# Kernel optimization log

Hardware: AMD Instinct MI355X
Metric: run time of the kernel (lower is better)

The kernel has to match this reference:

```python
import jax, jax.numpy as jnp
import numpy as np

B, S, H = 8, 2048, 1024
CHUNK = 64
INTER = 2048
BASE_LR = 0.01
MAX_GRAD_NORM = 1.0
EPS = 1e-6


def rmsnorm(x, w):
    return x * jax.lax.rsqrt(jnp.mean(x * x, axis=-1, keepdims=True) + EPS) * w


def mem_fwd(params, x):
    # 2-layer MLP memory with residual: x + RMSNorm(W1 @ silu(W0 @ x))
    w0, w1, ln = params
    h = jax.nn.silu(x @ w0.T)
    y = h @ w1.T
    return x + rmsnorm(y, ln)


def forward(x, wq_w, wk_w, wv_w, q_norm_w, k_norm_w, alpha_w, theta_w, eta_w, mem_w0, mem_w1, mem_ln_w):
    Bx, Sx, Hx = x.shape
    NC = Sx // CHUNK  # seq_len divisible by chunk_size here (no padding needed)
    xc = x.reshape(Bx, NC, CHUNK, Hx)
    xf = xc.reshape(Bx, NC, CHUNK * Hx)

    # adaptive coefficients per chunk
    alpha = jax.nn.sigmoid(jnp.mean(xf @ alpha_w.T, axis=0))   # (NC, 1)
    theta = jax.nn.sigmoid(xf @ theta_w.T) * BASE_LR           # (B, NC, 1) per-sample loss weights
    eta = jax.nn.sigmoid(jnp.mean(xf @ eta_w.T, axis=0))       # (NC, 1)
    beta = 1.0 - alpha

    k = rmsnorm(jax.nn.silu(xc @ wk_w.T), k_norm_w)  # (B, NC, C, H)
    v = jax.nn.silu(xc @ wv_w.T)                     # (B, NC, C, H)

    mem0 = (mem_w0, mem_w1, mem_ln_w)
    surp0 = jax.tree_util.tree_map(jnp.zeros_like, mem0)

    def step(carry, inp):
        mem, surp = carry
        k_c, v_c, th_c, eta_c, beta_c = inp  # k_c,v_c: (B,C,H); th_c: (B,1); eta_c,beta_c: (1,)

        def loss_fn(p):
            pred = mem_fwd(p, k_c)
            return jnp.mean((v_c - pred) ** 2 * th_c[:, :, None])

        grads = jax.grad(loss_fn)(mem)
        total = jnp.sqrt(sum(jnp.sum(g * g) for g in grads))
        clip = jax.lax.stop_gradient(jnp.minimum(MAX_GRAD_NORM / (total + 1e-6), 1.0))
        new_surp = tuple(eta_c * s_ - g * clip for s_, g in zip(surp, grads))
        new_mem = tuple(beta_c * m + ns for m, ns in zip(mem, new_surp))
        return (new_mem, new_surp), None

    xs = (jnp.swapaxes(k, 0, 1), jnp.swapaxes(v, 0, 1), jnp.swapaxes(theta, 0, 1), eta, beta)
    (mem_f, _), _ = jax.lax.scan(step, (mem0, surp0), xs)

    # retrieve with final memory weights
    q = rmsnorm(jax.nn.silu(x @ wq_w.T), q_norm_w)
    return mem_fwd(mem_f, q)


def setup_inputs() -> dict:
    key = jax.random.key(0)
    ks = jax.random.split(key, 9)
    s = 0.02
    return {
        "x": jax.random.normal(ks[0], (B, S, H), jnp.float32),
        "wq_w": jax.random.normal(ks[1], (H, H), jnp.float32) * s,
        "wk_w": jax.random.normal(ks[2], (H, H), jnp.float32) * s,
        "wv_w": jax.random.normal(ks[3], (H, H), jnp.float32) * s,
        "q_norm_w": jnp.ones((H,), jnp.float32),
        "k_norm_w": jnp.ones((H,), jnp.float32),
        "alpha_w": jax.random.normal(ks[4], (1, CHUNK * H), jnp.float32) * s,
        "theta_w": jax.random.normal(ks[5], (1, CHUNK * H), jnp.float32) * s,
        "eta_w": jax.random.normal(ks[6], (1, CHUNK * H), jnp.float32) * s,
        "mem_w0": jax.random.normal(ks[7], (INTER, H), jnp.float32) * s,
        "mem_w1": jax.random.normal(ks[8], (H, INTER), jnp.float32) * s,
        "mem_ln_w": jnp.ones((H,), jnp.float32),
    }


def reference(x, wq_w, wk_w, wv_w, q_norm_w, k_norm_w, alpha_w, theta_w, eta_w, mem_w0, mem_w1, mem_ln_w):
    return forward(x, wq_w, wk_w, wv_w, q_norm_w, k_norm_w, alpha_w, theta_w, eta_w, mem_w0, mem_w1, mem_ln_w)
```

## Files before the change

kernel.cpp:

```cpp
#include <hip/hip_runtime.h>

#define HD 1024
#define ID 2048
#define NCHUNK 32
#define CHUNKSZ 64
#define NB 8
#define SEQ 2048
#define ROWS 512
#define MTOT 524288.0f
#define EPSF 1e-6f

typedef unsigned short u16;
typedef unsigned int u32;
typedef short bf16x8 __attribute__((ext_vector_type(8)));
typedef float f32x4 __attribute__((ext_vector_type(4)));

#define GATHER(r, c) ((((r) >> 6) * SEQ) + ((c) * CHUNKSZ) + ((r) & 63))

__device__ __forceinline__ float sigmoidf_(float x) { return 1.f / (1.f + expf(-x)); }
__device__ __forceinline__ float siluf_(float x)    { return x / (1.f + expf(-x)); }
__device__ __forceinline__ float silu_d_(float z)   { float sg = sigmoidf_(z); return sg * (1.f + z * (1.f - sg)); }

__device__ __forceinline__ u16 f2b(float f) {
  union { float f; u32 u; } v; v.f = f;
  return (u16)((v.u + 0x7fffu + ((v.u >> 16) & 1u)) >> 16);
}
__device__ __forceinline__ float b2f(u16 b) {
  union { u32 u; float f; } v; v.u = ((u32)b) << 16; return v.f;
}
__device__ __forceinline__ u32 pack2(float a, float b) { return (u32)f2b(a) | ((u32)f2b(b) << 16); }

__device__ __forceinline__ float block_reduce_sum(float v, float* s4) {
  #pragma unroll
  for (int off = 32; off > 0; off >>= 1) v += __shfl_down(v, off);
  int lane = threadIdx.x & 63, wid = threadIdx.x >> 6;
  if (lane == 0) s4[wid] = v;
  __syncthreads();
  float r = s4[0] + s4[1] + s4[2] + s4[3];
  __syncthreads();
  return r;
}

template<bool T>
__device__ __forceinline__ void stage64(u16* S, int srow, int c16, const uint4& r0, const uint4& r1) {
  if (!T) {
    *(uint4*)(S + srow * 72 + c16)     = r0;
    *(uint4*)(S + srow * 72 + c16 + 8) = r1;
  } else {
    const u16* e0 = (const u16*)&r0;
    const u16* e1 = (const u16*)&r1;
    #pragma unroll
    for (int e = 0; e < 8; ++e) S[(c16 + e) * 72 + srow] = e0[e];
    #pragma unroll
    for (int e = 0; e < 8; ++e) S[(c16 + 8 + e) * 72 + srow] = e1[e];
  }
}

template<bool AT, bool BT>
__device__ __forceinline__ void gemm64_db(
    f32x4 (&acc)[2][2], const u16* __restrict__ A, const u16* __restrict__ B,
    int K, int m0, int n0, int lda, int ldb, int chA, int chB,
    u16* As, u16* Bs)
{
  const int tid = threadIdx.x;
  const int lane = tid & 63, wave = tid >> 6;
  const int wr = wave >> 1, wc = wave & 1;
  const int l15 = lane & 15, q = lane >> 4;
  const int srow = tid >> 2, c16 = (tid & 3) * 16;

  const u16* Ap; size_t Astep;
  if (!AT) {
    int r = m0 + srow;
    if (chA >= 0) r = GATHER(r, chA);
    Ap = A + (size_t)r * lda + c16;
    Astep = 64;
  } else {
    Ap = A + (size_t)srow * lda + m0 + c16;
    Astep = (size_t)64 * lda;
  }
  const u16* Bp; size_t Bstep;
  if (!BT) {
    Bp = B + (size_t)(n0 + srow) * ldb + c16;
    Bstep = 64;
  } else {
    if (chB >= 0) { Bp = B + ((size_t)chB * CHUNKSZ + srow) * ldb + n0 + c16; Bstep = (size_t)SEQ * ldb; }
    else          { Bp = B + (size_t)srow * ldb + n0 + c16;                   Bstep = (size_t)64 * ldb; }
  }

  uint4 ra0 = *(const uint4*)Ap, ra1 = *(const uint4*)(Ap + 8);
  uint4 rb0 = *(const uint4*)Bp, rb1 = *(const uint4*)(Bp + 8);
  stage64<AT>(As, srow, c16, ra0, ra1);
  stage64<BT>(Bs, srow, c16, rb0, rb1);

  const int nt = K >> 6;
  int cur = 0;
  for (int t = 0; t < nt; ++t) {
    if (t + 1 < nt) {
      Ap += Astep; Bp += Bstep;
      ra0 = *(const uint4*)Ap; ra1 = *(const uint4*)(Ap + 8);
      rb0 = *(const uint4*)Bp; rb1 = *(const uint4*)(Bp + 8);
    }
    __syncthreads();
    const u16* Ac = As + cur * (64 * 72);
    const u16* Bc = Bs + cur * (64 * 72);
    #pragma unroll
    for (int ks = 0; ks < 2; ++ks) {
      bf16x8 af[2], bg[2];
      #pragma unroll
      for (int i = 0; i < 2; ++i) af[i] = *(const bf16x8*)&Ac[(wr * 32 + i * 16 + l15) * 72 + ks * 32 + q * 8];
      #pragma unroll
      for (int j = 0; j < 2; ++j) bg[j] = *(const bf16x8*)&Bc[(wc * 32 + j * 16 + l15) * 72 + ks * 32 + q * 8];
      #pragma unroll
      for (int i = 0; i < 2; ++i)
        #pragma unroll
        for (int j = 0; j < 2; ++j)
          acc[i][j] = __builtin_amdgcn_mfma_f32_16x16x32_bf16(af[i], bg[j], acc[i][j], 0, 0, 0);
    }
    if (t + 1 < nt) {
      stage64<AT>(As + (cur ^ 1) * (64 * 72), srow, c16, ra0, ra1);
      stage64<BT>(Bs + (cur ^ 1) * (64 * 72), srow, c16, rb0, rb1);
    }
    cur ^= 1;
  }
}

template<bool BT>
__device__ __forceinline__ void gemm64x8(
    f32x4 (&acc)[2][2], const u16* __restrict__ A, const u16* __restrict__ B,
    int K, int m0, int n0, int lda, int ldb, int chA, u16* As, u16* Bs)
{
  const int tid = threadIdx.x;
  const int half = tid >> 8;
  const int t2 = tid & 255;
  const int lane = tid & 63;
  const int w2 = t2 >> 6;
  const int wr = w2 >> 1, wc = w2 & 1;
  const int l15 = lane & 15, q = lane >> 4;
  const int srow = t2 >> 2, c16 = (t2 & 3) * 16;
  const int kbase = half * (K >> 1);

  int arow = m0 + srow;
  if (chA >= 0) arow = GATHER(arow, chA);
  const u16* Ap = A + (size_t)arow * lda + kbase + c16;
  const u16* Bp; size_t Bstep;
  if (!BT) { Bp = B + (size_t)(n0 + srow) * ldb + kbase + c16; Bstep = 64; }
  else     { Bp = B + (size_t)(kbase + srow) * ldb + n0 + c16; Bstep = (size_t)64 * ldb; }

  u16* Ah = As + half * (2 * 64 * 72);
  u16* Bh = Bs + half * (2 * 64 * 72);

  uint4 ra0 = *(const uint4*)Ap, ra1 = *(const uint4*)(Ap + 8);
  uint4 rb0 = *(const uint4*)Bp, rb1 = *(const uint4*)(Bp + 8);
  stage64<false>(Ah, srow, c16, ra0, ra1);
  stage64<BT>(Bh, srow, c16, rb0, rb1);

  const int nt = K >> 7;
  int cur = 0;
  for (int t = 0; t < nt; ++t) {
    if (t + 1 < nt) {
      Ap += 64; Bp += Bstep;
      ra0 = *(const uint4*)Ap; ra1 = *(const uint4*)(Ap + 8);
      rb0 = *(const uint4*)Bp; rb1 = *(const uint4*)(Bp + 8);
    }
    __syncthreads();
    const u16* Ac = Ah + cur * (64 * 72);
    const u16* Bc = Bh + cur * (64 * 72);
    #pragma unroll
    for (int ks = 0; ks < 2; ++ks) {
      bf16x8 af[2], bg[2];
      #pragma unroll
      for (int i = 0; i < 2; ++i) af[i] = *(const bf16x8*)&Ac[(wr * 32 + i * 16 + l15) * 72 + ks * 32 + q * 8];
      #pragma unroll
      for (int j = 0; j < 2; ++j) bg[j] = *(const bf16x8*)&Bc[(wc * 32 + j * 16 + l15) * 72 + ks * 32 + q * 8];
      #pragma unroll
      for (int i = 0; i < 2; ++i)
        #pragma unroll
        for (int j = 0; j < 2; ++j)
          acc[i][j] = __builtin_amdgcn_mfma_f32_16x16x32_bf16(af[i], bg[j], acc[i][j], 0, 0, 0);
    }
    if (t + 1 < nt) {
      stage64<false>(Ah + (cur ^ 1) * (64 * 72), srow, c16, ra0, ra1);
      stage64<BT>(Bh + (cur ^ 1) * (64 * 72), srow, c16, rb0, rb1);
    }
    cur ^= 1;
  }
}

__global__ __launch_bounds__(512) void gemm64_fwd(
    float* __restrict__ C, u16* __restrict__ Cb,
    const u16* __restrict__ A, const u16* __restrict__ B, int N, int K, int chunk)
{
  __shared__ __align__(16) u16 As[2 * 2 * 64 * 72];
  __shared__ __align__(16) u16 Bs[2 * 2 * 64 * 72];
  const int m0 = blockIdx.y * 64, n0 = blockIdx.x * 64;
  f32x4 acc[2][2] = {};
  gemm64x8<false>(acc, A, B, K, m0, n0, K, K, chunk, As, Bs);
  const int tid = threadIdx.x;
  const int half = tid >> 8, t2 = tid & 255;
  const int lane = tid & 63, w2 = t2 >> 6;
  const int wr = w2 >> 1, wc = w2 & 1;
  const int l15 = lane & 15, q = lane >> 4;
  float* Cm = (float*)As;
  __syncthreads();
  if (half) {
    #pragma unroll
    for (int i = 0; i < 2; ++i)
      #pragma unroll
      for (int j = 0; j < 2; ++j)
        #pragma unroll
        for (int t = 0; t < 4; ++t)
          Cm[(wr * 32 + i * 16 + q * 4 + t) * 66 + wc * 32 + j * 16 + l15] = acc[i][j][t];
  }
  __syncthreads();
  if (!half) {
    #pragma unroll
    for (int i = 0; i < 2; ++i) {
      int r = m0 + wr * 32 + i * 16 + q * 4;
      #pragma unroll
      for (int j = 0; j < 2; ++j) {
        int col = n0 + wc * 32 + j * 16 + l15;
        #pragma unroll
        for (int t = 0; t < 4; ++t) {
          float v = acc[i][j][t] + Cm[(wr * 32 + i * 16 + q * 4 + t) * 66 + wc * 32 + j * 16 + l15];
          size_t o = (size_t)(r + t) * N + col;
          C[o] = v;
          Cb[o] = f2b(siluf_(v));
        }
      }
    }
  }
}

__global__ __launch_bounds__(512) void gemm64_dh(
    u16* __restrict__ Cb, const u16* __restrict__ A, const u16* __restrict__ B,
    const float* __restrict__ Z, int N, int K)
{
  __shared__ __align__(16) u16 As[2 * 2 * 64 * 72];
  __shared__ __align__(16) u16 Bs[2 * 2 * 64 * 72];
  const int m0 = blockIdx.y * 64, n0 = blockIdx.x * 64;
  f32x4 acc[2][2] = {};
  gemm64x8<true>(acc, A, B, K, m0, n0, K, N, -1, As, Bs);
  const int tid = threadIdx.x;
  const int half = tid >> 8, t2 = tid & 255;
  const int lane = tid & 63, w2 = t2 >> 6;
  const int wr = w2 >> 1, wc = w2 & 1;
  const int l15 = lane & 15, q = lane >> 4;
  float* Cm = (float*)As;
  __syncthreads();
  if (half) {
    #pragma unroll
    for (int i = 0; i < 2; ++i)
      #pragma unroll
      for (int j = 0; j < 2; ++j)
        #pragma unroll
        for (int t = 0; t < 4; ++t)
          Cm[(wr * 32 + i * 16 + q * 4 + t) * 66 + wc * 32 + j * 16 + l15] = acc[i][j][t];
  }
  __syncthreads();
  if (!half) {
    #pragma unroll
    for (int i = 0; i < 2; ++i) {
      int r = m0 + wr * 32 + i * 16 + q * 4;
      #pragma unroll
      for (int j = 0; j < 2; ++j) {
        int col = n0 + wc * 32 + j * 16 + l15;
        #pragma unroll
        for (int t = 0; t < 4; ++t) {
          float v = acc[i][j][t] + Cm[(wr * 32 + i * 16 + q * 4 + t) * 66 + wc * 32 + j * 16 + l15];
          size_t o = (size_t)(r + t) * N + col;
          Cb[o] = f2b(v * silu_d_(Z[o]));
        }
      }
    }
  }
}

__global__ __launch_bounds__(256) void gemm_grads(
    float* __restrict__ Gw1, const u16* __restrict__ dY, const u16* __restrict__ hfw,
    float* __restrict__ Gw0, const u16* __restrict__ dH, const u16* __restrict__ kall,
    int c, const float* __restrict__ g, const float* __restrict__ y,
    const float* __restrict__ srow, float* __restrict__ Gln, float* __restrict__ nsqc)
{
  __shared__ __align__(16) u16 As[2 * 64 * 72];
  __shared__ __align__(16) u16 Bs[2 * 64 * 72];
  __shared__ float s4[4];
  int bid = blockIdx.x;
  const int tid = threadIdx.x;
  if (bid >= 1024) {
    int j = (bid - 1024) * 32 + (tid & 31);
    int rg = tid >> 5;
    float acc = 0.f;
    #pragma unroll 4
    for (int i = 0; i < 64; ++i) {
      int r = rg * 64 + i;
      size_t o = (size_t)r * HD + j;
      acc += g[o] * y[o] * srow[r];
    }
    float* part = (float*)As;
    part[rg * 32 + (tid & 31)] = acc;
    __syncthreads();
    if (tid < 32) {
      float tot = 0.f;
      #pragma unroll
      for (int k = 0; k < 8; ++k) tot += part[k * 32 + tid];
      Gln[j] = tot;
      float sq = tot * tot;
      #pragma unroll
      for (int off = 16; off > 0; off >>= 1) sq += __shfl_down(sq, off);
      if (tid == 0) atomicAdd(nsqc, sq);
    }
    return;
  }
  float* C; const u16* A; const u16* B; int N, m0, n0, lda, ldb, chB;
  if (bid < 512) { A = dY; B = hfw;  C = Gw1; N = ID; lda = HD; ldb = ID; chB = -1; m0 = (bid >> 5) * 64; n0 = (bid & 31) * 64; }
  else { bid -= 512; A = dH; B = kall; C = Gw0; N = HD; lda = ID; ldb = HD; chB = c; m0 = (bid >> 4) * 64; n0 = (bid & 15) * 64; }
  f32x4 acc[2][2] = {};
  gemm64_db<true, true>(acc, A, B, ROWS, m0, n0, lda, ldb, -1, chB, As, Bs);
  const int lane = tid & 63, wave = tid >> 6;
  const int wr = wave >> 1, wc = wave & 1;
  const int l15 = lane & 15, q = lane >> 4;
  float ssq = 0.f;
  #pragma unroll
  for (int i = 0; i < 2; ++i) {
    int r = m0 + wr * 32 + i * 16 + q * 4;
    #pragma unroll
    for (int j = 0; j < 2; ++j) {
      int col = n0 + wc * 32 + j * 16 + l15;
      #pragma unroll
      for (int t = 0; t < 4; ++t) {
        float v = acc[i][j][t];
        C[(size_t)(r + t) * N + col] = v;
        ssq += v * v;
      }
    }
  }
  float tot = block_reduce_sum(ssq, s4);
  if (tid == 0) atomicAdd(nsqc, tot);
}

__global__ __launch_bounds__(512) void gemm_y32(
    float* __restrict__ C, const u16* __restrict__ A, const u16* __restrict__ B,
    int N, int K)
{
  __shared__ __align__(16) u16 As[4 * 2 * 32 * 72];
  __shared__ __align__(16) u16 Bs[4 * 2 * 64 * 72];
  const int tid = threadIdx.x;
  const int qt = tid >> 7;
  const int t2 = tid & 127;
  const int lane = tid & 63;
  const int wc = t2 >> 6;
  const int l15 = lane & 15, q = lane >> 4;
  const int m0 = blockIdx.y * 32, n0 = blockIdx.x * 64;
  const int kbase = qt * (K >> 2);

  const int arow = t2 >> 2, ac16 = (t2 & 3) * 16;
  const int brow = t2 >> 1, bc32 = (t2 & 1) * 32;
  const u16* Ap = A + (size_t)(m0 + arow) * K + kbase + ac16;
  const u16* Bp = B + (size_t)(n0 + brow) * K + kbase + bc32;
  u16* Aq = As + qt * (2 * 32 * 72);
  u16* Bq = Bs + qt * (2 * 64 * 72);

  uint4 ra0 = *(const uint4*)Ap, ra1 = *(const uint4*)(Ap + 8);
  uint4 rb0 = *(const uint4*)Bp, rb1 = *(const uint4*)(Bp + 8);
  uint4 rb2 = *(const uint4*)(Bp + 16), rb3 = *(const uint4*)(Bp + 24);
  {
    u16* Aw = Aq + arow * 72 + ac16;
    u16* Bw = Bq + brow * 72 + bc32;
    *(uint4*)Aw = ra0; *(uint4*)(Aw + 8) = ra1;
    *(uint4*)Bw = rb0; *(uint4*)(Bw + 8) = rb1;
    *(uint4*)(Bw + 16) = rb2; *(uint4*)(Bw + 24) = rb3;
  }

  f32x4 acc[2][2] = {};
  const int nt = K >> 8;
  int cur = 0;
  for (int t = 0; t < nt; ++t) {
    if (t + 1 < nt) {
      Ap += 64; Bp += 64;
      ra0 = *(const uint4*)Ap; ra1 = *(const uint4*)(Ap + 8);
      rb0 = *(const uint4*)Bp; rb1 = *(const uint4*)(Bp + 8);
      rb2 = *(const uint4*)(Bp + 16); rb3 = *(const uint4*)(Bp + 24);
    }
    __syncthreads();
    const u16* Ac = Aq + cur * (32 * 72);
    const u16* Bc = Bq + cur * (64 * 72);
    #pragma unroll
    for (int ks = 0; ks < 2; ++ks) {
      bf16x8 af[2], bg[2];
      #pragma unroll
      for (int i = 0; i < 2; ++i) af[i] = *(const bf16x8*)&Ac[(i * 16 + l15) * 72 + ks * 32 + q * 8];
      #pragma unroll
      for (int j = 0; j < 2; ++j) bg[j] = *(const bf16x8*)&Bc[(wc * 32 + j * 16 + l15) * 72 + ks * 32 + q * 8];
      #pragma unroll
      for (int i = 0; i < 2; ++i)
        #pragma unroll
        for (int j = 0; j < 2; ++j)
          acc[i][j] = __builtin_amdgcn_mfma_f32_16x16x32_bf16(af[i], bg[j], acc[i][j], 0, 0, 0);
    }
    if (t + 1 < nt) {
      u16* Aw = Aq + (cur ^ 1) * (32 * 72) + arow * 72 + ac16;
      u16* Bw = Bq + (cur ^ 1) * (64 * 72) + brow * 72 + bc32;
      *(uint4*)Aw = ra0; *(uint4*)(Aw + 8) = ra1;
      *(uint4*)Bw = rb0; *(uint4*)(Bw + 8) = rb1;
      *(uint4*)(Bw + 16) = rb2; *(uint4*)(Bw + 24) = rb3;
    }
    cur ^= 1;
  }
  float* Cm = (float*)As;
  __syncthreads();
  if (qt) {
    #pragma unroll
    for (int i = 0; i < 2; ++i)
      #pragma unroll
      for (int j = 0; j < 2; ++j)
        #pragma unroll
        for (int t = 0; t < 4; ++t)
          Cm[((qt - 1) * 32 + i * 16 + q * 4 + t) * 66 + wc * 32 + j * 16 + l15] = acc[i][j][t];
  }
  __syncthreads();
  if (!qt) {
    #pragma unroll
    for (int i = 0; i < 2; ++i) {
      int r = m0 + i * 16 + q * 4;
      #pragma unroll
      for (int j = 0; j < 2; ++j) {
        int col = n0 + wc * 32 + j * 16 + l15;
        #pragma unroll
        for (int t = 0; t < 4; ++t) {
          float v = acc[i][j][t];
          #pragma unroll
          for (int p = 0; p < 3; ++p)
            v += Cm[(p * 32 + i * 16 + q * 4 + t) * 66 + wc * 32 + j * 16 + l15];
          C[(size_t)(r + t) * N + col] = v;
        }
      }
    }
  }
}

__device__ __forceinline__ void gemm128_core(
    f32x4 (&acc)[4][4], const u16* __restrict__ A, int lda,
    const u16* __restrict__ B, int ldb, int K, int m0, int n0,
    u16* As, u16* Bs)
{
  const int tid = threadIdx.x;
  const int lane = tid & 63, wave = tid >> 6;
  const int wr = wave >> 1, wc = wave & 1;
  const int l15 = lane & 15, q = lane >> 4;
  for (int k0 = 0; k0 < K; k0 += 32) {
    #pragma unroll
    for (int it = 0; it < 2; ++it) {
      int cid = tid + it * 256;
      int row = cid >> 2, c8 = (cid & 3) * 8;
      *(uint4*)&As[row * 40 + c8] = *(const uint4*)&A[(size_t)(m0 + row) * lda + k0 + c8];
      *(uint4*)&Bs[row * 40 + c8] = *(const uint4*)&B[(size_t)(n0 + row) * ldb + k0 + c8];
    }
    __syncthreads();
    bf16x8 af[4], bg[4];
    #pragma unroll
    for (int i = 0; i < 4; ++i) af[i] = *(const bf16x8*)&As[(wr * 64 + i * 16 + l15) * 40 + q * 8];
    #pragma unroll
    for (int j = 0; j < 4; ++j) bg[j] = *(const bf16x8*)&Bs[(wc * 64 + j * 16 + l15) * 40 + q * 8];
    #pragma unroll
    for (int i = 0; i < 4; ++i)
      #pragma unroll
      for (int j = 0; j < 4; ++j)
        acc[i][j] = __builtin_amdgcn_mfma_f32_16x16x32_bf16(af[i], bg[j], acc[i][j], 0, 0, 0);
    __syncthreads();
  }
}

__global__ __launch_bounds__(256) void gemm_qkv(
    float* __restrict__ zqC, u16* __restrict__ kC, u16* __restrict__ vC,
    const u16* __restrict__ xb, const u16* __restrict__ wk,
    const u16* __restrict__ wv, const u16* __restrict__ wq)
{
  __shared__ __align__(16) u16 As[128 * 40];
  __shared__ __align__(16) u16 Bs[128 * 40];
  int f = blockIdx.x;
  int xcd = f & 7, jj = f >> 3;
  int panel = xcd + 8 * (jj / 24);
  int w = jj % 24;
  int z = w >> 3, xt = w & 7;
  int m0 = panel * 128, n0 = xt * 128;
  const u16* B = (z == 0) ? wk : ((z == 1) ? wv : wq);
  f32x4 acc[4][4] = {};
  gemm128_core(acc, xb, HD, B, HD, HD, m0, n0, As, Bs);
  const int tid = threadIdx.x;
  const int lane = tid & 63, wave = tid >> 6;
  const int wr = wave >> 1, wc = wave & 1;
  const int l15 = lane & 15, q = lane >> 4;
  #pragma unroll
  for (int i = 0; i < 4; ++i) {
    int r = m0 + wr * 64 + i * 16 + q * 4;
    #pragma unroll
    for (int j = 0; j < 4; ++j) {
      int col = n0 + wc * 64 + j * 16 + l15;
      #pragma unroll
      for (int t = 0; t < 4; ++t) {
        float v = acc[i][j][t];
        size_t o = (size_t)(r + t) * HD + col;
        if (z == 0) kC[o] = f2b(v);
        else if (z == 1) vC[o] = f2b(siluf_(v));
        else zqC[o] = v;
      }
    }
  }
}

__global__ __launch_bounds__(256) void gemm_h(
    u16* __restrict__ hC, const u16* __restrict__ A, const u16* __restrict__ B)
{
  __shared__ __align__(16) u16 As[128 * 40];
  __shared__ __align__(16) u16 Bs[128 * 40];
  int f = blockIdx.x;
  int xcd = f & 7, jj = f >> 3;
  int panel = xcd + 8 * (jj >> 4);
  int xt = jj & 15;
  int m0 = panel * 128, n0 = xt * 128;
  f32x4 acc[4][4] = {};
  gemm128_core(acc, A, HD, B, HD, HD, m0, n0, As, Bs);
  const int tid = threadIdx.x;
  const int lane = tid & 63, wave = tid >> 6;
  const int wr = wave >> 1, wc = wave & 1;
  const int l15 = lane & 15, q = lane >> 4;
  #pragma unroll
  for (int i = 0; i < 4; ++i) {
    int r = m0 + wr * 64 + i * 16 + q * 4;
    #pragma unroll
    for (int j = 0; j < 4; ++j) {
      int col = n0 + wc * 64 + j * 16 + l15;
      #pragma unroll
      for (int t = 0; t < 4; ++t)
        hC[(size_t)(r + t) * ID + col] = f2b(siluf_(acc[i][j][t]));
    }
  }
}

__global__ __launch_bounds__(256) void gemm_y2(
    float* __restrict__ C, const u16* __restrict__ A, const u16* __restrict__ B)
{
  __shared__ __align__(16) u16 As[128 * 40];
  __shared__ __align__(16) u16 Bs[128 * 40];
  int f = blockIdx.x;
  int xcd = f & 7, jj = f >> 3;
  int panel = xcd + 8 * (jj >> 3);
  int xt = jj & 7;
  int m0 = panel * 128, n0 = xt * 128;
  f32x4 acc[4][4] = {};
  gemm128_core(acc, A, ID, B, ID, ID, m0, n0, As, Bs);
  const int tid = threadIdx.x;
  const int lane = tid & 63, wave = tid >> 6;
  const int wr = wave >> 1, wc = wave & 1;
  const int l15 = lane & 15, q = lane >> 4;
  #pragma unroll
  for (int i = 0; i < 4; ++i) {
    int r = m0 + wr * 64 + i * 16 + q * 4;
    #pragma unroll
    for (int j = 0; j < 4; ++j) {
      int col = n0 + wc * 64 + j * 16 + l15;
      #pragma unroll
      for (int t = 0; t < 4; ++t)
        C[(size_t)(r + t) * HD + col] = acc[i][j][t];
    }
  }
}

__global__ __launch_bounds__(256) void conv_f2b(u16* __restrict__ dst, const float* __restrict__ src, int n) {
  int i = (blockIdx.x * 256 + threadIdx.x) * 4;
  if (i < n) {
    float4 v = *(const float4*)&src[i];
    uint2 o; o.x = pack2(v.x, v.y); o.y = pack2(v.z, v.w);
    *(uint2*)&dst[i] = o;
  }
}

__global__ __launch_bounds__(256) void dots_kernel(
    const float* __restrict__ x, const float* __restrict__ aw,
    const float* __restrict__ tw, const float* __restrict__ ew,
    float* __restrict__ dA, float* __restrict__ dT, float* __restrict__ dE)
{
  int b = blockIdx.x >> 5, c = blockIdx.x & 31;
  const float* base = x + ((size_t)b * SEQ + (size_t)c * CHUNKSZ) * HD;
  float a = 0.f, t = 0.f, e = 0.f;
  for (int it = 0; it < 64; ++it) {
    int j = (it * 256 + threadIdx.x) * 4;
    float4 xv = *(const float4*)&base[j];
    float4 av = *(const float4*)&aw[j];
    float4 tv = *(const float4*)&tw[j];
    float4 ev = *(const float4*)&ew[j];
    a += xv.x * av.x + xv.y * av.y + xv.z * av.z + xv.w * av.w;
    t += xv.x * tv.x + xv.y * tv.y + xv.z * tv.z + xv.w * tv.w;
    e += xv.x * ev.x + xv.y * ev.y + xv.z * ev.z + xv.w * ev.w;
  }
  __shared__ float s4[4];
  a = block_reduce_sum(a, s4);
  t = block_reduce_sum(t, s4);
  e = block_reduce_sum(e, s4);
  if (threadIdx.x == 0) { dA[blockIdx.x] = a; dT[blockIdx.x] = t; dE[blockIdx.x] = e; }
}

__global__ __launch_bounds__(256) void coeff_kernel(
    const float* __restrict__ dA, const float* __restrict__ dT, const float* __restrict__ dE,
    float* __restrict__ betaA, float* __restrict__ etaA, float* __restrict__ thetaA)
{
  int t = threadIdx.x;
  if (t < 256) thetaA[t] = sigmoidf_(dT[t]) * 0.01f;
  if (t < 32) {
    float sa = 0.f, se = 0.f;
    for (int b = 0; b < NB; ++b) { sa += dA[b * 32 + t]; se += dE[b * 32 + t]; }
    betaA[t] = 1.f - sigmoidf_(sa / 8.f);
    etaA[t]  = sigmoidf_(se / 8.f);
  }
}

__global__ __launch_bounds__(256) void post_norm_kb(u16* buf, const float* __restrict__ nw)
{
  size_t off = (size_t)blockIdx.x * HD;
  float sv[4]; float ss = 0.f;
  #pragma unroll
  for (int i = 0; i < 4; ++i) {
    int j = i * 256 + threadIdx.x;
    float s = siluf_(b2f(buf[off + j]));
    sv[i] = s; ss += s * s;
  }
  __shared__ float s4[4];
  ss = block_reduce_sum(ss, s4);
  float rs = rsqrtf(ss / (float)HD + EPSF);
  #pragma unroll
  for (int i = 0; i < 4; ++i) {
    int j = i * 256 + threadIdx.x;
    buf[off + j] = f2b(sv[i] * rs * nw[j]);
  }
}

__global__ __launch_bounds__(256) void post_norm_qf(float* buf, const float* __restrict__ nw)
{
  size_t off = (size_t)blockIdx.x * HD;
  float sv[4]; float ss = 0.f;
  #pragma unroll
  for (int i = 0; i < 4; ++i) {
    int j = i * 256 + threadIdx.x;
    float s = siluf_(buf[off + j]);
    sv[i] = s; ss += s * s;
  }
  __shared__ float s4[4];
  ss = block_reduce_sum(ss, s4);
  float rs = rsqrtf(ss / (float)HD + EPSF);
  #pragma unroll
  for (int i = 0; i < 4; ++i) {
    int j = i * 256 + threadIdx.x;
    buf[off + j] = sv[i] * rs * nw[j];
  }
}

__global__ __launch_bounds__(256) void loss_grad(
    const float* __restrict__ y, const u16* __restrict__ kall, const u16* __restrict__ vall,
    const float* __restrict__ ln, const float* __restrict__ thetaA, int c,
    float* __restrict__ g, u16* __restrict__ dYbf, float* __restrict__ srow)
{
  int r = blockIdx.x;
  size_t off = (size_t)r * HD;
  size_t goff = (size_t)GATHER(r, c) * HD;
  float th = thetaA[(r >> 6) * 32 + c];
  float yv[4], lnv[4];
  float ss = 0.f;
  #pragma unroll
  for (int i = 0; i < 4; ++i) {
    int j = i * 256 + threadIdx.x;
    yv[i] = y[off + j];
    lnv[i] = ln[j];
    ss += yv[i] * yv[i];
  }
  __shared__ float s4[4];
  ss = block_reduce_sum(ss, s4);
  float s = rsqrtf(ss / (float)HD + EPSF);
  float coef = 2.f * th / MTOT;
  float gv[4]; float t = 0.f;
  #pragma unroll
  for (int i = 0; i < 4; ++i) {
    int j = i * 256 + threadIdx.x;
    float pred = b2f(kall[goff + j]) + yv[i] * s * lnv[i];
    float gg = coef * (pred - b2f(vall[goff + j]));
    gv[i] = gg;
    g[off + j] = gg;
    t += gg * lnv[i] * yv[i];
  }
  t = block_reduce_sum(t, s4);
  float c3 = s * s * s * t * (1.f / (float)HD);
  #pragma unroll
  for (int i = 0; i < 4; ++i) {
    int j = i * 256 + threadIdx.x;
    dYbf[off + j] = f2b(s * gv[i] * lnv[i] - c3 * yv[i]);
  }
  if (threadIdx.x == 0) srow[r] = s;
}

__global__ __launch_bounds__(256) void update_all(
    float* __restrict__ mw0, float* __restrict__ sw0, const float* __restrict__ g0, u16* __restrict__ w0b,
    float* __restrict__ mw1, float* __restrict__ sw1, const float* __restrict__ g1, u16* __restrict__ w1b,
    float* __restrict__ mln, float* __restrict__ sln, const float* __restrict__ gl,
    const float* __restrict__ etaA, const float* __restrict__ betaA, int c,
    const float* __restrict__ nsqc)
{
  float clip = fminf(1.0f / (sqrtf(*nsqc) + 1e-6f), 1.0f);
  float eta = etaA[c], beta = betaA[c];
  int bid = blockIdx.x;
  if (bid < 2048) {
    float* mw; float* sw; const float* g; u16* wb; size_t i0;
    if (bid < 1024) { mw = mw1; sw = sw1; g = g1; wb = w1b; i0 = (size_t)bid * 2048; }
    else            { mw = mw0; sw = sw0; g = g0; wb = w0b; i0 = (size_t)(bid - 1024) * 2048; }
    i0 += (size_t)threadIdx.x * 8;
    u16 bb[8];
    #pragma unroll
    for (int h = 0; h < 2; ++h) {
      size_t i = i0 + h * 4;
      float4 s = *(float4*)&sw[i];
      float4 gg = *(const float4*)&g[i];
      float4 m = *(float4*)&mw[i];
      s.x = eta * s.x - clip * gg.x; m.x = beta * m.x + s.x;
      s.y = eta * s.y - clip * gg.y; m.y = beta * m.y + s.y;
      s.z = eta * s.z - clip * gg.z; m.z = beta * m.z + s.z;
      s.w = eta * s.w - clip * gg.w; m.w = beta * m.w + s.w;
      *(float4*)&sw[i] = s;
      *(float4*)&mw[i] = m;
      bb[h * 4 + 0] = f2b(m.x); bb[h * 4 + 1] = f2b(m.y);
      bb[h * 4 + 2] = f2b(m.z); bb[h * 4 + 3] = f2b(m.w);
    }
    *(uint4*)&wb[i0] = *(uint4*)bb;
  } else {
    int i = threadIdx.x * 4;
    #pragma unroll
    for (int k = 0; k < 4; ++k) {
      float ns = eta * sln[i + k] - clip * gl[i + k];
      sln[i + k] = ns;
      mln[i + k] = beta * mln[i + k] + ns;
    }
  }
}

__global__ __launch_bounds__(256) void final_out_kernel(
    float* outp, const float* __restrict__ y2, const float* __restrict__ ln)
{
  size_t off = (size_t)blockIdx.x * HD;
  float qv[4], yv[4];
  float ss2 = 0.f;
  #pragma unroll
  for (int i = 0; i < 4; ++i) {
    int j = i * 256 + threadIdx.x;
    qv[i] = outp[off + j];
    yv[i] = y2[off + j];
    ss2 += yv[i] * yv[i];
  }
  __shared__ float s4[4];
  ss2 = block_reduce_sum(ss2, s4);
  float rs2 = rsqrtf(ss2 / (float)HD + EPSF);
  #pragma unroll
  for (int i = 0; i < 4; ++i) {
    int j = i * 256 + threadIdx.x;
    outp[off + j] = qv[i] + yv[i] * rs2 * ln[j];
  }
}

extern "C" void kernel_launch(void* const* d_in, const int* in_sizes, int n_in,
                              void* d_out, int out_size, void* d_ws, size_t ws_size,
                              hipStream_t stream) {
  const float* x   = (const float*)d_in[0];
  const float* wq  = (const float*)d_in[1];
  const float* wk  = (const float*)d_in[2];
  const float* wv  = (const float*)d_in[3];
  const float* qn  = (const float*)d_in[4];
  const float* kn  = (const float*)d_in[5];
  const float* aw  = (const float*)d_in[6];
  const float* tw  = (const float*)d_in[7];
  const float* ew  = (const float*)d_in[8];
  const float* w0i = (const float*)d_in[9];
  const float* w1i = (const float*)d_in[10];
  const float* lni = (const float*)d_in[11];
  float* out = (float*)d_out;

  float* p = (float*)d_ws;
  auto alloc = [&](size_t n) { n = (n + 63) & ~(size_t)63; float* r = p; p += n; return r; };
  float* memW0  = alloc((size_t)ID * HD);
  float* memW1  = alloc((size_t)HD * ID);
  float* surpW0 = alloc((size_t)ID * HD);
  float* surpW1 = alloc((size_t)HD * ID);
  float* Gw0    = alloc((size_t)ID * HD);
  float* Gw1    = alloc((size_t)HD * ID);
  float* memLn  = alloc(HD);
  float* surpLn = alloc(HD);
  float* Gln    = alloc(HD);
  float* zfw    = alloc((size_t)ROWS * ID);
  float* ybuf   = alloc((size_t)ROWS * HD);
  float* gbuf   = alloc((size_t)ROWS * HD);
  float* srow   = alloc(ROWS);
  float* dotA   = alloc(256);
  float* dotT   = alloc(256);
  float* dotE   = alloc(256);
  float* betaA  = alloc(64);
  float* etaA   = alloc(64);
  float* thetaA = alloc(256);
  float* nsq    = alloc(64);

  u16* bp = (u16*)p;
  auto balloc = [&](size_t n) { n = (n + 63) & ~(size_t)63; u16* r = bp; bp += n; return r; };
  u16* wq_bf  = balloc((size_t)HD * HD);
  u16* wk_bf  = balloc((size_t)HD * HD);
  u16* wv_bf  = balloc((size_t)HD * HD);
  u16* W0_bf  = balloc((size_t)ID * HD);
  u16* W1_bf  = balloc((size_t)HD * ID);
  u16* k_all  = balloc((size_t)NB * SEQ * HD);
  u16* v_all  = balloc((size_t)NB * SEQ * HD);
  u16* hfw_bf = balloc((size_t)ROWS * ID);
  u16* dY_bf  = balloc((size_t)ROWS * HD);
  u16* dH_bf  = balloc((size_t)ROWS * ID);
  size_t needed = (size_t)((char*)bp - (char*)d_ws);
  if (needed > ws_size) return;

  u16* x_bf = (u16*)memW0;

  conv_f2b<<<(HD * HD) / 1024, 256, 0, stream>>>(wq_bf, wq, HD * HD);
  conv_f2b<<<(HD * HD) / 1024, 256, 0, stream>>>(wk_bf, wk, HD * HD);
  conv_f2b<<<(HD * HD) / 1024, 256, 0, stream>>>(wv_bf, wv, HD * HD);
  conv_f2b<<<(ID * HD) / 1024, 256, 0, stream>>>(W0_bf, w0i, ID * HD);
  conv_f2b<<<(HD * ID) / 1024, 256, 0, stream>>>(W1_bf, w1i, HD * ID);
  conv_f2b<<<(NB * SEQ * HD) / 1024, 256, 0, stream>>>(x_bf, x, NB * SEQ * HD);
  dots_kernel<<<256, 256, 0, stream>>>(x, aw, tw, ew, dotA, dotT, dotE);
  coeff_kernel<<<1, 256, 0, stream>>>(dotA, dotT, dotE, betaA, etaA, thetaA);
  gemm_qkv<<<3072, 256, 0, stream>>>(out, k_all, v_all, x_bf, wk_bf, wv_bf, wq_bf);
  post_norm_kb<<<NB * SEQ, 256, 0, stream>>>(k_all, kn);
  post_norm_qf<<<NB * SEQ, 256, 0, stream>>>(out, qn);
  hipMemcpyAsync(memW0, w0i, (size_t)ID * HD * 4, hipMemcpyDeviceToDevice, stream);
  hipMemcpyAsync(memW1, w1i, (size_t)HD * ID * 4, hipMemcpyDeviceToDevice, stream);
  hipMemcpyAsync(memLn, lni, (size_t)HD * 4, hipMemcpyDeviceToDevice, stream);
  hipMemsetAsync(surpW0, 0, (size_t)ID * HD * 2 * 4, stream);
  hipMemsetAsync(surpLn, 0, HD * 4, stream);
  hipMemsetAsync(nsq, 0, 64 * 4, stream);

  for (int c = 0; c < NCHUNK; ++c) {
    gemm64_fwd<<<dim3(ID / 64, ROWS / 64), 512, 0, stream>>>(
        zfw, hfw_bf, k_all, W0_bf, ID, HD, c);
    gemm_y32<<<dim3(HD / 64, ROWS / 32), 512, 0, stream>>>(ybuf, hfw_bf, W1_bf, HD, ID);
    loss_grad<<<ROWS, 256, 0, stream>>>(ybuf, k_all, v_all, memLn, thetaA, c, gbuf, dY_bf, srow);
    gemm64_dh<<<dim3(ID / 64, ROWS / 64), 512, 0, stream>>>(
        dH_bf, dY_bf, W1_bf, zfw, ID, HD);
    gemm_grads<<<1056, 256, 0, stream>>>(
        Gw1, dY_bf, hfw_bf, Gw0, dH_bf, k_all, c, gbuf, ybuf, srow, Gln, nsq + c);
    update_all<<<2049, 256, 0, stream>>>(
        memW0, surpW0, Gw0, W0_bf, memW1, surpW1, Gw1, W1_bf,
        memLn, surpLn, Gln, etaA, betaA, c, nsq + c);
  }

  u16*   qb_bf = k_all;
  u16*   h_bf  = v_all;
  float* y2    = surpW0;
  conv_f2b<<<(NB * SEQ * HD) / 1024, 256, 0, stream>>>(qb_bf, out, NB * SEQ * HD);
  for (int blk = 0; blk < 2; ++blk) {
    gemm_h<<<1024, 256, 0, stream>>>(h_bf, qb_bf + (size_t)blk * 8192 * HD, W0_bf);
    gemm_y2<<<512, 256, 0, stream>>>(y2, h_bf, W1_bf);
    final_out_kernel<<<8192, 256, 0, stream>>>(out + (size_t)blk * 8192 * HD, y2, memLn);
  }
}
```

Measured before the change: 3.106 ms.

## Double-buffer 128-tile GEMM core and remap transposed staging thread layout

Replaces the single-buffered 128x128 GEMM core used by the qkv, h and y2 kernels with a register-prefetched, double-buffered LDS pipeline. This overlaps the global loads for the next K tile with the MFMA work and drops one barrier per iteration. It also changes the thread-to-element mapping in the transposed staging paths of the 64-tile GEMMs so each thread owns one k-row, which changes the LDS scatter bank pattern. LDS use doubles for the 128-tile kernels, which may lower occupancy.

After: 3.221 ms. 3.7% more time.

```diff
diff --git a/kernel.cpp b/kernel.cpp
--- a/kernel.cpp
+++ b/kernel.cpp
@@ -41,56 +41,34 @@
   return r;
 }
 
-template<bool T>
-__device__ __forceinline__ void stage64(u16* S, int srow, int c16, const uint4& r0, const uint4& r1) {
-  if (!T) {
-    *(uint4*)(S + srow * 72 + c16)     = r0;
-    *(uint4*)(S + srow * 72 + c16 + 8) = r1;
-  } else {
-    const u16* e0 = (const u16*)&r0;
-    const u16* e1 = (const u16*)&r1;
-    #pragma unroll
-    for (int e = 0; e < 8; ++e) S[(c16 + e) * 72 + srow] = e0[e];
-    #pragma unroll
-    for (int e = 0; e < 8; ++e) S[(c16 + 8 + e) * 72 + srow] = e1[e];
-  }
-}
-
-template<bool AT, bool BT>
-__device__ __forceinline__ void gemm64_db(
+__device__ __forceinline__ void gemm64_tn(
     f32x4 (&acc)[2][2], const u16* __restrict__ A, const u16* __restrict__ B,
-    int K, int m0, int n0, int lda, int ldb, int chA, int chB,
-    u16* As, u16* Bs)
+    int K, int m0, int n0, int lda, int ldb, int chB, u16* As, u16* Bs)
 {
   const int tid = threadIdx.x;
   const int lane = tid & 63, wave = tid >> 6;
   const int wr = wave >> 1, wc = wave & 1;
   const int l15 = lane & 15, q = lane >> 4;
-  const int srow = tid >> 2, c16 = (tid & 3) * 16;
-
-  const u16* Ap; size_t Astep;
-  if (!AT) {
-    int r = m0 + srow;
-    if (chA >= 0) r = GATHER(r, chA);
-    Ap = A + (size_t)r * lda + c16;
-    Astep = 64;
-  } else {
-    Ap = A + (size_t)srow * lda + m0 + c16;
-    Astep = (size_t)64 * lda;
-  }
+  const int kr = tid & 63, cg = (tid >> 6) * 16;
+
+  const u16* Ap = A + (size_t)kr * lda + m0 + cg;
+  const size_t Astep = (size_t)64 * lda;
   const u16* Bp; size_t Bstep;
-  if (!BT) {
-    Bp = B + (size_t)(n0 + srow) * ldb + c16;
-    Bstep = 64;
-  } else {
-    if (chB >= 0) { Bp = B + ((size_t)chB * CHUNKSZ + srow) * ldb + n0 + c16; Bstep = (size_t)SEQ * ldb; }
-    else          { Bp = B + (size_t)srow * ldb + n0 + c16;                   Bstep = (size_t)64 * ldb; }
-  }
+  if (chB >= 0) { Bp = B + ((size_t)chB * CHUNKSZ + kr) * ldb + n0 + cg; Bstep = (size_t)SEQ * ldb; }
+  else          { Bp = B + (size_t)kr * ldb + n0 + cg;                   Bstep = (size_t)64 * ldb; }
+
+  auto scat = [&](u16* S, const uint4& r0, const uint4& r1) {
+    const u16* e0 = (const u16*)&r0; const u16* e1 = (const u16*)&r1;
+    #pragma unroll
+    for (int e = 0; e < 8; ++e) S[(cg + e) * 72 + kr] = e0[e];
+    #pragma unroll
+    for (int e = 0; e < 8; ++e) S[(cg + 8 + e) * 72 + kr] = e1[e];
+  };
 
   uint4 ra0 = *(const uint4*)Ap, ra1 = *(const uint4*)(Ap + 8);
   uint4 rb0 = *(const uint4*)Bp, rb1 = *(const uint4*)(Bp + 8);
-  stage64<AT>(As, srow, c16, ra0, ra1);
-  stage64<BT>(Bs, srow, c16, rb0, rb1);
+  scat(As, ra0, ra1);
+  scat(Bs, rb0, rb1);
 
   const int nt = K >> 6;
   int cur = 0;
@@ -117,8 +95,8 @@
           acc[i][j] = __builtin_amdgcn_mfma_f32_16x16x32_bf16(af[i], bg[j], acc[i][j], 0, 0, 0);
     }
     if (t + 1 < nt) {
-      stage64<AT>(As + (cur ^ 1) * (64 * 72), srow, c16, ra0, ra1);
-      stage64<BT>(Bs + (cur ^ 1) * (64 * 72), srow, c16, rb0, rb1);
+      scat(As + (cur ^ 1) * (64 * 72), ra0, ra1);
+      scat(Bs + (cur ^ 1) * (64 * 72), rb0, rb1);
     }
     cur ^= 1;
   }
@@ -137,6 +115,7 @@
   const int wr = w2 >> 1, wc = w2 & 1;
   const int l15 = lane & 15, q = lane >> 4;
   const int srow = t2 >> 2, c16 = (t2 & 3) * 16;
+  const int kr = t2 & 63, cg = (t2 >> 6) * 16;
   const int kbase = half * (K >> 1);
 
   int arow = m0 + srow;
@@ -144,15 +123,32 @@
   const u16* Ap = A + (size_t)arow * lda + kbase + c16;
   const u16* Bp; size_t Bstep;
   if (!BT) { Bp = B + (size_t)(n0 + srow) * ldb + kbase + c16; Bstep = 64; }
-  else     { Bp = B + (size_t)(kbase + srow) * ldb + n0 + c16; Bstep = (size_t)64 * ldb; }
+  else     { Bp = B + (size_t)(kbase + kr) * ldb + n0 + cg;    Bstep = (size_t)64 * ldb; }
 
   u16* Ah = As + half * (2 * 64 * 72);
   u16* Bh = Bs + half * (2 * 64 * 72);
 
+  auto stA = [&](u16* S, const uint4& r0, const uint4& r1) {
+    *(uint4*)(S + srow * 72 + c16)     = r0;
+    *(uint4*)(S + srow * 72 + c16 + 8) = r1;
+  };
+  auto stB = [&](u16* S, const uint4& r0, const uint4& r1) {
+    if (!BT) {
+      *(uint4*)(S + srow * 72 + c16)     = r0;
+      *(uint4*)(S + srow * 72 + c16 + 8) = r1;
+    } else {
+      const u16* e0 = (const u16*)&r0; const u16* e1 = (const u16*)&r1;
+      #pragma unroll
+      for (int e = 0; e < 8; ++e) S[(cg + e) * 72 + kr] = e0[e];
+      #pragma unroll
+      for (int e = 0; e < 8; ++e) S[(cg + 8 + e) * 72 + kr] = e1[e];
+    }
+  };
+
   uint4 ra0 = *(const uint4*)Ap, ra1 = *(const uint4*)(Ap + 8);
   uint4 rb0 = *(const uint4*)Bp, rb1 = *(const uint4*)(Bp + 8);
-  stage64<false>(Ah, srow, c16, ra0, ra1);
-  stage64<BT>(Bh, srow, c16, rb0, rb1);
+  stA(Ah, ra0, ra1);
+  stB(Bh, rb0, rb1);
 
   const int nt = K >> 7;
   int cur = 0;
@@ -179,8 +175,8 @@
           acc[i][j] = __builtin_amdgcn_mfma_f32_16x16x32_bf16(af[i], bg[j], acc[i][j], 0, 0, 0);
     }
     if (t + 1 < nt) {
-      stage64<false>(Ah + (cur ^ 1) * (64 * 72), srow, c16, ra0, ra1);
-      stage64<BT>(Bh + (cur ^ 1) * (64 * 72), srow, c16, rb0, rb1);
+      stA(Ah + (cur ^ 1) * (64 * 72), ra0, ra1);
+      stB(Bh + (cur ^ 1) * (64 * 72), rb0, rb1);
     }
     cur ^= 1;
   }
@@ -315,7 +311,7 @@
   if (bid < 512) { A = dY; B = hfw;  C = Gw1; N = ID; lda = HD; ldb = ID; chB = -1; m0 = (bid >> 5) * 64; n0 = (bid & 31) * 64; }
   else { bid -= 512; A = dH; B = kall; C = Gw0; N = HD; lda = ID; ldb = HD; chB = c; m0 = (bid >> 4) * 64; n0 = (bid & 15) * 64; }
   f32x4 acc[2][2] = {};
-  gemm64_db<true, true>(acc, A, B, ROWS, m0, n0, lda, ldb, -1, chB, As, Bs);
+  gemm64_tn(acc, A, B, ROWS, m0, n0, lda, ldb, chB, As, Bs);
   const int lane = tid & 63, wave = tid >> 6;
   const int wr = wave >> 1, wc = wave & 1;
   const int l15 = lane & 15, q = lane >> 4;
@@ -438,7 +434,7 @@
   }
 }
 
-__device__ __forceinline__ void gemm128_core(
+__device__ __forceinline__ void gemm128_db(
     f32x4 (&acc)[4][4], const u16* __restrict__ A, int lda,
     const u16* __restrict__ B, int ldb, int K, int m0, int n0,
     u16* As, u16* Bs)
@@ -447,26 +443,50 @@
   const int lane = tid & 63, wave = tid >> 6;
   const int wr = wave >> 1, wc = wave & 1;
   const int l15 = lane & 15, q = lane >> 4;
-  for (int k0 = 0; k0 < K; k0 += 32) {
-    #pragma unroll
-    for (int it = 0; it < 2; ++it) {
-      int cid = tid + it * 256;
-      int row = cid >> 2, c8 = (cid & 3) * 8;
-      *(uint4*)&As[row * 40 + c8] = *(const uint4*)&A[(size_t)(m0 + row) * lda + k0 + c8];
-      *(uint4*)&Bs[row * 40 + c8] = *(const uint4*)&B[(size_t)(n0 + row) * ldb + k0 + c8];
+  const int row0 = tid >> 2, c8 = (tid & 3) * 8;
+
+  const u16* Ap0 = A + (size_t)(m0 + row0) * lda + c8;
+  const u16* Ap1 = Ap0 + (size_t)64 * lda;
+  const u16* Bp0 = B + (size_t)(n0 + row0) * ldb + c8;
+  const u16* Bp1 = Bp0 + (size_t)64 * ldb;
+
+  uint4 a0 = *(const uint4*)Ap0, a1 = *(const uint4*)Ap1;
+  uint4 b0 = *(const uint4*)Bp0, b1 = *(const uint4*)Bp1;
+  *(uint4*)&As[row0 * 40 + c8] = a0;
+  *(uint4*)&As[(row0 + 64) * 40 + c8] = a1;
+  *(uint4*)&Bs[row0 * 40 + c8] = b0;
+  *(uint4*)&Bs[(row0 + 64) * 40 + c8] = b1;
+
+  const int nt = K >> 5;
+  int cur = 0;
+  for (int t = 0; t < nt; ++t) {
+    if (t + 1 < nt) {
+      int k1 = (t + 1) * 32;
+      a0 = *(const uint4*)(Ap0 + k1); a1 = *(const uint4*)(Ap1 + k1);
+      b0 = *(const uint4*)(Bp0 + k1); b1 = *(const uint4*)(Bp1 + k1);
     }
     __syncthreads();
+    const u16* Ac = As + cur * (128 * 40);
+    const u16* Bc = Bs + cur * (128 * 40);
     bf16x8 af[4], bg[4];
     #pragma unroll
-    for (int i = 0; i < 4; ++i) af[i] = *(const bf16x8*)&As[(wr * 64 + i * 16 + l15) * 40 + q * 8];
-    #pragma unroll
-    for (int j = 0; j < 4; ++j) bg[j] = *(const bf16x8*)&Bs[(wc * 64 + j * 16 + l15) * 40 + q * 8];
+    for (int i = 0; i < 4; ++i) af[i] = *(const bf16x8*)&Ac[(wr * 64 + i * 16 + l15) * 40 + q * 8];
+    #pragma unroll
+    for (int j = 0; j < 4; ++j) bg[j] = *(const bf16x8*)&Bc[(wc * 64 + j * 16 + l15) * 40 + q * 8];
     #pragma unroll
     for (int i = 0; i < 4; ++i)
       #pragma unroll
       for (int j = 0; j < 4; ++j)
         acc[i][j] = __builtin_amdgcn_mfma_f32_16x16x32_bf16(af[i], bg[j], acc[i][j], 0, 0, 0);
-    __syncthreads();
+    if (t + 1 < nt) {
+      u16* Aw = As + (cur ^ 1) * (128 * 40);
+      u16* Bw = Bs + (cur ^ 1) * (128 * 40);
+      *(uint4*)&Aw[row0 * 40 + c8] = a0;
+      *(uint4*)&Aw[(row0 + 64) * 40 + c8] = a1;
+      *(uint4*)&Bw[row0 * 40 + c8] = b0;
+      *(uint4*)&Bw[(row0 + 64) * 40 + c8] = b1;
+    }
+    cur ^= 1;
   }
 }
 
@@ -475,8 +495,8 @@
     const u16* __restrict__ xb, const u16* __restrict__ wk,
     const u16* __restrict__ wv, const u16* __restrict__ wq)
 {
-  __shared__ __align__(16) u16 As[128 * 40];
-  __shared__ __align__(16) u16 Bs[128 * 40];
+  __shared__ __align__(16) u16 As[2 * 128 * 40];
+  __shared__ __align__(16) u16 Bs[2 * 128 * 40];
   int f = blockIdx.x;
   int xcd = f & 7, jj = f >> 3;
   int panel = xcd + 8 * (jj / 24);
@@ -485,7 +505,7 @@
   int m0 = panel * 128, n0 = xt * 128;
   const u16* B = (z == 0) ? wk : ((z == 1) ? wv : wq);
   f32x4 acc[4][4] = {};
-  gemm128_core(acc, xb, HD, B, HD, HD, m0, n0, As, Bs);
+  gemm128_db(acc, xb, HD, B, HD, HD, m0, n0, As, Bs);
   const int tid = threadIdx.x;
   const int lane = tid & 63, wave = tid >> 6;
   const int wr = wave >> 1, wc = wave & 1;
@@ -511,15 +531,15 @@
 __global__ __launch_bounds__(256) void gemm_h(
     u16* __restrict__ hC, const u16* __restrict__ A, const u16* __restrict__ B)
 {
-  __shared__ __align__(16) u16 As[128 * 40];
-  __shared__ __align__(16) u16 Bs[128 * 40];
+  __shared__ __align__(16) u16 As[2 * 128 * 40];
+  __shared__ __align__(16) u16 Bs[2 * 128 * 40];
   int f = blockIdx.x;
   int xcd = f & 7, jj = f >> 3;
   int panel = xcd + 8 * (jj >> 4);
   int xt = jj & 15;
   int m0 = panel * 128, n0 = xt * 128;
   f32x4 acc[4][4] = {};
-  gemm128_core(acc, A, HD, B, HD, HD, m0, n0, As, Bs);
+  gemm128_db(acc, A, HD, B, HD, HD, m0, n0, As, Bs);
   const int tid = threadIdx.x;
   const int lane = tid & 63, wave = tid >> 6;
   const int wr = wave >> 1, wc = wave & 1;
@@ -540,15 +560,15 @@
 __global__ __launch_bounds__(256) void gemm_y2(
     float* __restrict__ C, const u16* __restrict__ A, const u16* __restrict__ B)
 {
-  __shared__ __align__(16) u16 As[128 * 40];
-  __shared__ __align__(16) u16 Bs[128 * 40];
+  __shared__ __align__(16) u16 As[2 * 128 * 40];
+  __shared__ __align__(16) u16 Bs[2 * 128 * 40];
   int f = blockIdx.x;
   int xcd = f & 7, jj = f >> 3;
   int panel = xcd + 8 * (jj >> 3);
   int xt = jj & 7;
   int m0 = panel * 128, n0 = xt * 128;
   f32x4 acc[4][4] = {};
-  gemm128_core(acc, A, ID, B, ID, ID, m0, n0, As, Bs);
+  gemm128_db(acc, A, ID, B, ID, ID, m0, n0, As, Bs);
   const int tid = threadIdx.x;
   const int lane = tid & 63, wave = tid >> 6;
   const int wr = wave >> 1, wc = wave & 1;
```
